# Optimization experiments

Hardware: AMD Instinct MI355X
Metric: run time of the kernel (lower is better)

Reference implementation:

```python
import jax, jax.numpy as jnp
import numpy as np

T, B, D = 1024, 16, 1024
BETA_INIT = 2.0


def _beta_gemm(beta_param, t):
    # beta = sigmoid(raw param); lower-triangular matrix M[i, j] = beta**(i-j) for j <= i
    beta = jax.nn.sigmoid(beta_param)
    i = jnp.arange(t)[:, None]
    j = jnp.arange(t)[None, :]
    expo = i - j                      # [T, T]
    mask = expo >= 0
    # clamp exponent in masked-out region to avoid inf from negative powers
    mat = beta ** jnp.where(mask, expo, 0).astype(beta.dtype)
    return jnp.where(mask, mat, jnp.zeros((), beta.dtype))


def setup_inputs() -> dict:
    key = jax.random.key(0)
    k1, _ = jax.random.split(key)
    x_seq = jax.random.normal(k1, (T, B, D), dtype=jnp.float32)
    beta_param = jnp.asarray(BETA_INIT, dtype=jnp.float32)
    return {"x_seq": x_seq, "beta_param": beta_param}


def reference(x_seq, beta_param):
    t = x_seq.shape[0]
    beta_gemm = _beta_gemm(beta_param, t)            # [T, T] lower-tri decay
    flat = x_seq.reshape(t, -1)                       # [T, B*D]
    y = beta_gemm @ flat                              # addmm with zero bias
    return y.reshape(x_seq.shape)
```

## Files before the change

### kernel.cpp

```cpp
#include <hip/hip_runtime.h>
#include <math.h>

#define T_DIM 1024
#define C_DIM 16384
#define WAVES 16
#define BLOCK_T (WAVES * 64)
#define L_CHUNK (T_DIM / WAVES)

__global__ __launch_bounds__(BLOCK_T, 4)
void pli_scan_kernel(const float* __restrict__ x,
                     const float* __restrict__ beta_p,
                     float* __restrict__ out) {
    const int lane = threadIdx.x & 63;
    const int w    = threadIdx.x >> 6;
    const int col  = (blockIdx.x << 6) + lane;

    const float beta = 1.0f / (1.0f + expf(-beta_p[0]));

    const size_t base = (size_t)(w * L_CHUNK) * C_DIM + col;
    const float* xp = x + base;

    float v[L_CHUNK];
#pragma unroll
    for (int t = 0; t < L_CHUNK; ++t) {
        v[t] = xp[(size_t)t * C_DIM];
    }

    float run = 0.0f;
#pragma unroll
    for (int t = 0; t < L_CHUNK; ++t) {
        run = fmaf(run, beta, v[t]);
        v[t] = run;
    }

    __shared__ float carry[WAVES][64];
    carry[w][lane] = run;
    __syncthreads();

    float bL = beta;
#pragma unroll
    for (int i = 0; i < 6; ++i) bL *= bL;

    float Y = 0.0f;
    for (int u = 0; u < w; ++u) {
        Y = fmaf(Y, bL, carry[u][lane]);
    }

    float m = beta * Y;
    float* op = out + base;
#pragma unroll
    for (int t = 0; t < L_CHUNK; ++t) {
        op[(size_t)t * C_DIM] = v[t] + m;
        m *= beta;
    }
}

extern "C" void kernel_launch(void* const* d_in, const int* in_sizes, int n_in,
                              void* d_out, int out_size, void* d_ws, size_t ws_size,
                              hipStream_t stream) {
    const float* x      = (const float*)d_in[0];
    const float* beta_p = (const float*)d_in[1];
    float* out          = (float*)d_out;

    dim3 grid(C_DIM / 64);
    dim3 block(BLOCK_T);
    hipLaunchKernelGGL(pli_scan_kernel, grid, block, 0, stream, x, beta_p, out);
}
```

Measured before the change: 111.5 us.

## Split scan into carry and apply kernels with float4 column tiles

Replaces the single-block chunked scan with two kernels. The first computes per-chunk decayed carries for 4-wide column groups into workspace. The second combines the prior carries and rescans each chunk, writing output. This aims to use vectorized loads and remove the large per-thread register array and block-wide sync. The cost is that x is read twice and there is an extra launch and workspace traffic.

```diff
diff --git a/kernel.cpp b/kernel.cpp
--- a/kernel.cpp
+++ b/kernel.cpp
@@ -1,57 +1,74 @@
 #include <hip/hip_runtime.h>
 #include <math.h>
 
-#define T_DIM 1024
-#define C_DIM 16384
-#define WAVES 16
-#define BLOCK_T (WAVES * 64)
-#define L_CHUNK (T_DIM / WAVES)
+#define T_DIM    1024
+#define C_DIM    16384
+#define CHUNKS   16
+#define LROWS    64
+#define COLTILES 16
+#define TILE_COLS 1024
+#define NTHREADS 256
 
-__global__ __launch_bounds__(BLOCK_T, 4)
-void pli_scan_kernel(const float* __restrict__ x,
-                     const float* __restrict__ beta_p,
-                     float* __restrict__ out) {
-    const int lane = threadIdx.x & 63;
-    const int w    = threadIdx.x >> 6;
-    const int col  = (blockIdx.x << 6) + lane;
+__device__ __forceinline__ float sigmoid_(float v) {
+    return 1.0f / (1.0f + expf(-v));
+}
 
-    const float beta = 1.0f / (1.0f + expf(-beta_p[0]));
+__global__ __launch_bounds__(NTHREADS, 4)
+void k1_carries(const float* __restrict__ x,
+                const float* __restrict__ beta_p,
+                float* __restrict__ carry) {
+    const int tile = blockIdx.x & (COLTILES - 1);
+    const int c    = blockIdx.x >> 4;
+    const int col  = tile * TILE_COLS + (threadIdx.x << 2);
+    const float beta = sigmoid_(beta_p[0]);
 
-    const size_t base = (size_t)(w * L_CHUNK) * C_DIM + col;
-    const float* xp = x + base;
+    const float4* xp = (const float4*)(x + (size_t)(c * LROWS) * C_DIM + col);
+    float4 run = make_float4(0.f, 0.f, 0.f, 0.f);
+#pragma unroll 16
+    for (int t = 0; t < LROWS; ++t) {
+        float4 v = xp[(size_t)t * (C_DIM / 4)];
+        run.x = fmaf(run.x, beta, v.x);
+        run.y = fmaf(run.y, beta, v.y);
+        run.z = fmaf(run.z, beta, v.z);
+        run.w = fmaf(run.w, beta, v.w);
+    }
+    *(float4*)(carry + (size_t)c * C_DIM + col) = run;
+}
 
-    float v[L_CHUNK];
-#pragma unroll
-    for (int t = 0; t < L_CHUNK; ++t) {
-        v[t] = xp[(size_t)t * C_DIM];
-    }
-
-    float run = 0.0f;
-#pragma unroll
-    for (int t = 0; t < L_CHUNK; ++t) {
-        run = fmaf(run, beta, v[t]);
-        v[t] = run;
-    }
-
-    __shared__ float carry[WAVES][64];
-    carry[w][lane] = run;
-    __syncthreads();
+__global__ __launch_bounds__(NTHREADS, 4)
+void k2_apply(const float* __restrict__ x,
+              const float* __restrict__ beta_p,
+              const float* __restrict__ carry,
+              float* __restrict__ out) {
+    const int tile = blockIdx.x & (COLTILES - 1);
+    const int c    = blockIdx.x >> 4;
+    const int col  = tile * TILE_COLS + (threadIdx.x << 2);
+    const float beta = sigmoid_(beta_p[0]);
 
     float bL = beta;
 #pragma unroll
     for (int i = 0; i < 6; ++i) bL *= bL;
 
-    float Y = 0.0f;
-    for (int u = 0; u < w; ++u) {
-        Y = fmaf(Y, bL, carry[u][lane]);
+    float4 Y = make_float4(0.f, 0.f, 0.f, 0.f);
+    for (int u = 0; u < c; ++u) {
+        float4 cv = *(const float4*)(carry + (size_t)u * C_DIM + col);
+        Y.x = fmaf(Y.x, bL, cv.x);
+        Y.y = fmaf(Y.y, bL, cv.y);
+        Y.z = fmaf(Y.z, bL, cv.z);
+        Y.w = fmaf(Y.w, bL, cv.w);
     }
 
-    float m = beta * Y;
-    float* op = out + base;
-#pragma unroll
-    for (int t = 0; t < L_CHUNK; ++t) {
-        op[(size_t)t * C_DIM] = v[t] + m;
-        m *= beta;
+    const float4* xp = (const float4*)(x + (size_t)(c * LROWS) * C_DIM + col);
+    float4*       op = (float4*)(out + (size_t)(c * LROWS) * C_DIM + col);
+    float4 run = Y;
+#pragma unroll 16
+    for (int t = 0; t < LROWS; ++t) {
+        float4 v = xp[(size_t)t * (C_DIM / 4)];
+        run.x = fmaf(run.x, beta, v.x);
+        run.y = fmaf(run.y, beta, v.y);
+        run.z = fmaf(run.z, beta, v.z);
+        run.w = fmaf(run.w, beta, v.w);
+        op[(size_t)t * (C_DIM / 4)] = run;
     }
 }
 
@@ -61,8 +78,10 @@
     const float* x      = (const float*)d_in[0];
     const float* beta_p = (const float*)d_in[1];
     float* out          = (float*)d_out;
+    float* carry        = (float*)d_ws;
 
-    dim3 grid(C_DIM / 64);
-    dim3 block(BLOCK_T);
-    hipLaunchKernelGGL(pli_scan_kernel, grid, block, 0, stream, x, beta_p, out);
+    dim3 grid(COLTILES * CHUNKS);
+    dim3 block(NTHREADS);
+    hipLaunchKernelGGL(k1_carries, grid, block, 0, stream, x, beta_p, carry);
+    hipLaunchKernelGGL(k2_apply,   grid, block, 0, stream, x, beta_p, carry, out);
 }
```

New measurement: 125.4 us. +12.4%, slower.
